# Optimization experiments

Measured on AMD Instinct MI355X. Metric: run time of the kernel, lower is better.

## Reference

```python
import jax, jax.numpy as jnp
import numpy as np

D_MODEL = 1024
NUM_HEADS = 16
HEAD_DIM = D_MODEL // NUM_HEADS
B, T = 4, 2048


def setup_inputs() -> dict:
    key = jax.random.key(0)
    ks = jax.random.split(key, 11)
    s = 0.02
    return {
        "q": jax.random.normal(ks[0], (B, T, D_MODEL), jnp.float32),
        "k": jax.random.normal(ks[1], (B, T, D_MODEL), jnp.float32),
        "v": jax.random.normal(ks[2], (B, T, D_MODEL), jnp.float32),
        "Wq": jax.random.normal(ks[3], (D_MODEL, D_MODEL), jnp.float32) * s,
        "bq": jnp.zeros((D_MODEL,), jnp.float32),
        "Wk": jax.random.normal(ks[4], (D_MODEL, D_MODEL), jnp.float32) * s,
        "bk": jnp.zeros((D_MODEL,), jnp.float32),
        "Wv": jax.random.normal(ks[5], (D_MODEL, D_MODEL), jnp.float32) * s,
        "bv": jnp.zeros((D_MODEL,), jnp.float32),
        "Wo": jax.random.normal(ks[6], (D_MODEL, D_MODEL), jnp.float32) * s,
        "bo": jnp.zeros((D_MODEL,), jnp.float32),
    }


def reference(q, k, v, Wq, bq, Wk, bk, Wv, bv, Wo, bo):
    Bq, Tq, _ = q.shape
    Tk = k.shape[1]
    # Linear projections then split heads: [B, H, T, Dh]
    qh = (q @ Wq + bq).reshape(Bq, Tq, NUM_HEADS, HEAD_DIM).transpose(0, 2, 1, 3)
    kh = (k @ Wk + bk).reshape(Bq, Tk, NUM_HEADS, HEAD_DIM).transpose(0, 2, 1, 3)
    vh = (v @ Wv + bv).reshape(Bq, Tk, NUM_HEADS, HEAD_DIM).transpose(0, 2, 1, 3)
    scale = 1.0 / jnp.sqrt(jnp.asarray(HEAD_DIM, qh.dtype))
    scores = jnp.einsum("bhqd,bhkd->bhqk", qh, kh) * scale  # [B,H,Tq,Tk]
    attn = jax.nn.softmax(scores, axis=-1)
    # dropout p=0.0 (eval) -> identity
    out = jnp.einsum("bhqk,bhkd->bhqd", attn, vh)  # [B,H,Tq,Dh]
    out = out.transpose(0, 2, 1, 3).reshape(Bq, Tq, D_MODEL)
    return out @ Wo + bo
```

## Files before the change

### kernel.cpp

```cpp
#include <hip/hip_runtime.h>
#include <cstdint>

#define DEV static __device__ __forceinline__

typedef unsigned short u16;
typedef unsigned int u32;
typedef __attribute__((ext_vector_type(8))) _Float16 half8;
typedef __attribute__((ext_vector_type(4))) float f32x4;
typedef __attribute__((ext_vector_type(4))) unsigned short u16x4;

DEV u16 f2h_bits(float f) {
  _Float16 h = (_Float16)f;
  union { _Float16 h; u16 u; } cv; cv.h = h; return cv.u;
}

DEV u32 pack2h(float a, float b) {
  union { __fp16 __attribute__((ext_vector_type(2))) h; u32 u; } cv;
  cv.h = __builtin_amdgcn_cvt_pkrtz(a, b);
  return cv.u;
}

#define EXP2 __builtin_amdgcn_exp2f

DEV void async_cp16(const void* g, void* l) {
  __builtin_amdgcn_global_load_lds(
      (const __attribute__((address_space(1))) void*)g,
      (__attribute__((address_space(3))) void*)l, 16, 0, 0);
}

__global__ void cvt_f16(const float4* __restrict__ in, u16* __restrict__ out) {
  const int i = blockIdx.x * 256 + threadIdx.x;
  float4 f = in[i];
  u16x4 u;
  u.x = f2h_bits(f.x); u.y = f2h_bits(f.y); u.z = f2h_bits(f.z); u.w = f2h_bits(f.w);
  *(u16x4*)(out + i * 4) = u;
}

struct TParams { const float* W[4]; u16* out[4]; };

__global__ void tcvt4(TParams p) {
  __shared__ float tile[32][33];
  const int w = blockIdx.x >> 10;
  const int bidx = blockIdx.x & 1023;
  const float* __restrict__ Wf = p.W[w];
  u16* __restrict__ Wt = p.out[w];
  const int bx = bidx & 31, by = bidx >> 5;
  const int tx = threadIdx.x & 31, ty = threadIdx.x >> 5;
#pragma unroll
  for (int r = 0; r < 32; r += 8)
    tile[ty + r][tx] = Wf[(by * 32 + ty + r) * 1024 + bx * 32 + tx];
  __syncthreads();
#pragma unroll
  for (int r = 0; r < 32; r += 8)
    Wt[(bx * 32 + ty + r) * 1024 + by * 32 + tx] = f2h_bits(tile[tx][ty + r]);
}

template<int EPI, typename OutT>
DEV void gemm_body(const u16* __restrict__ A, const u16* __restrict__ Bt,
                   const float* __restrict__ bias, OutT* __restrict__ out,
                   u16 (*As)[8192], u16 (*Bs)[8192])
{
  const int tid = threadIdx.x;
  const int wave = tid >> 6, lane = tid & 63;
  const int l15 = lane & 15, lg = lane >> 4;
  const int bid = ((blockIdx.x & 7) << 6) | (blockIdx.x >> 3);
  const int bm = bid >> 3, bn = bid & 7;
  const int m0 = bm * 128, n0 = bn * 128;
  const int wr = wave >> 1, wc = wave & 1;

  const f32x4 fz = {0.f, 0.f, 0.f, 0.f};
  f32x4 acc[4][4];
#pragma unroll
  for (int m = 0; m < 4; ++m)
#pragma unroll
    for (int n = 0; n < 4; ++n) acc[m][n] = fz;

  const char* srcA[4]; const char* srcB[4]; int dstAB[4];
#pragma unroll
  for (int j = 0; j < 4; ++j) {
    const int x = (j * 256 + tid) * 16;
    const int row = x >> 7, colb = x & 127;
    const int pc = colb ^ ((row & 7) << 4);
    srcA[j] = (const char*)A  + (size_t)(m0 + row) * 2048 + pc;
    srcB[j] = (const char*)Bt + (size_t)(n0 + row) * 2048 + pc;
    dstAB[j] = x;
  }

#define STAGE_G(buf, T)                                                     \
  do {                                                                      \
    _Pragma("unroll") for (int j = 0; j < 4; ++j)                           \
      async_cp16(srcA[j] + (size_t)(T) * 128, (char*)As[buf] + dstAB[j]);   \
    _Pragma("unroll") for (int j = 0; j < 4; ++j)                           \
      async_cp16(srcB[j] + (size_t)(T) * 128, (char*)Bs[buf] + dstAB[j]);   \
  } while (0)

  STAGE_G(0, 0);
  asm volatile("s_waitcnt vmcnt(0)" ::: "memory");
  __builtin_amdgcn_s_barrier();
  __builtin_amdgcn_sched_barrier(0);

#define GEMM_IT(T, BR, BS)                                                  \
  do {                                                                      \
    if ((T) < 15) STAGE_G(BS, (T) + 1);                                     \
    half8 af[2][4], bf[2][4];                                               \
    _Pragma("unroll") for (int kk = 0; kk < 2; ++kk)                        \
      _Pragma("unroll") for (int m = 0; m < 4; ++m) {                       \
        const int row = wr * 64 + m * 16 + l15;                             \
        af[kk][m] = *(const half8*)((const char*)As[BR] +                   \
            ((row * 128 + kk * 64 + lg * 16) ^ ((row & 7) << 4)));          \
      }                                                                     \
    _Pragma("unroll") for (int kk = 0; kk < 2; ++kk)                        \
      _Pragma("unroll") for (int n = 0; n < 4; ++n) {                       \
        const int row = wc * 64 + n * 16 + l15;                             \
        bf[kk][n] = *(const half8*)((const char*)Bs[BR] +                   \
            ((row * 128 + kk * 64 + lg * 16) ^ ((row & 7) << 4)));          \
      }                                                                     \
    _Pragma("unroll") for (int kk = 0; kk < 2; ++kk)                        \
      _Pragma("unroll") for (int m = 0; m < 4; ++m)                         \
        _Pragma("unroll") for (int n = 0; n < 4; ++n)                       \
          acc[m][n] = __builtin_amdgcn_mfma_f32_16x16x32_f16(af[kk][m], bf[kk][n], acc[m][n], 0, 0, 0); \
    if ((T) < 15) {                                                         \
      asm volatile("s_waitcnt vmcnt(0)" ::: "memory");                      \
      __builtin_amdgcn_s_barrier();                                         \
      __builtin_amdgcn_sched_barrier(0);                                    \
    }                                                                       \
  } while (0)

  for (int tb = 0; tb < 16; tb += 2) {
    GEMM_IT(tb,     0, 1);
    GEMM_IT(tb + 1, 1, 0);
  }
#undef GEMM_IT
#undef STAGE_G

#pragma unroll
  for (int m = 0; m < 4; ++m) {
    const int Rb = m0 + wr * 64 + m * 16 + lg * 4;
#pragma unroll
    for (int n = 0; n < 4; ++n) {
      const int C = n0 + wc * 64 + n * 16 + l15;
      const float bv = bias[C];
#pragma unroll
      for (int i = 0; i < 4; ++i) {
        const int R = Rb + i;
        const float vv = acc[m][n][i] + bv;
        if (EPI == 3) {
          ((float*)out)[(size_t)R * 1024 + C] = vv;
        } else {
          const int b = R >> 11, t = R & 2047, hh = C >> 6, d = C & 63;
          if (EPI == 0)
            ((u16*)out)[((b * 16 + hh) * 2048 + t) * 64 + d] = f2h_bits(vv * 0.18033688f);
          else if (EPI == 1)
            ((u16*)out)[((b * 16 + hh) * 2048 + t) * 64 + d] = f2h_bits(vv);
          else
            ((u16*)out)[((b * 16 + hh) * 64 + d) * 2048 + t] = f2h_bits(vv);
        }
      }
    }
  }
}

template<int EPI>
__launch_bounds__(256, 2)
__global__ void gemm_proj(const u16* __restrict__ A, const u16* __restrict__ Bt,
                          const float* __restrict__ bias, u16* __restrict__ out)
{
  __shared__ u16 As[2][8192];
  __shared__ u16 Bs[2][8192];
  gemm_body<EPI, u16>(A, Bt, bias, out, As, Bs);
}

__launch_bounds__(256, 2)
__global__ void gemm_o(const u16* __restrict__ A, const u16* __restrict__ Bt,
                       const float* __restrict__ bias, float* __restrict__ out)
{
  __shared__ u16 As[2][8192];
  __shared__ u16 Bs[2][8192];
  gemm_body<3, float>(A, Bt, bias, out, As, Bs);
}

__launch_bounds__(512)
__global__ void attn_kernel(const u16* __restrict__ qh, const u16* __restrict__ kh,
                            const u16* __restrict__ vt, u16* __restrict__ O)
{
  __shared__ u16 SM[16384];
  const int tid = threadIdx.x, wave = tid >> 6, lane = tid & 63;
  const int l15 = lane & 15, lg = lane >> 4;
  const int swz = ((blockIdx.x & 7) << 6) | (blockIdx.x >> 3);
  const int bh = swz >> 3;
  const int q0 = (swz & 7) << 8;
  const int b = bh >> 4, h = bh & 15;

  const char* qbase = (const char*)(qh + (size_t)(bh * 2048 + q0) * 64);
  const char* kbase = (const char*)(kh + (size_t)bh * 2048 * 64);
  const char* vbase = (const char*)(vt + (size_t)bh * 64 * 2048);

  char* Kbuf[2] = { (char*)SM,         (char*)SM + 8192 };
  char* Vbuf[2] = { (char*)SM + 16384, (char*)SM + 24576 };

  const bool isK = wave < 4;
  const char* ksrc[2]; int kdst[2];
  const char* vsrc[2]; int vdstA[2], vdstB[2];
#pragma unroll
  for (int j = 0; j < 2; ++j) {
    if (isK) {
      const int yb = wave * 2048 + j * 1024 + lane * 16;
      const int row = yb >> 7;
      ksrc[j] = kbase + (yb ^ ((row & 7) << 4));
      kdst[j] = yb;
      vsrc[j] = nullptr; vdstA[j] = vdstB[j] = 0;
    } else {
      const int u = (wave - 4) * 128 + j * 64 + lane;
      const int d = u >> 3, a = u & 7;
      vsrc[j] = vbase + (size_t)d * 4096 + a * 16;
      const int n = a >> 1;
      const int s1 = 32 * (n >> 1) + 16 * (a & 1) + 4 * (n & 1);
      const int sw = (d & 7) << 4;
      vdstA[j] = (d * 128 + 2 * s1) ^ sw;
      vdstB[j] = (d * 128 + 2 * s1 + 16) ^ sw;
      ksrc[j] = nullptr; kdst[j] = 0;
    }
  }

#pragma unroll
  for (int j = 0; j < 4; ++j) {
    const int x = j * 8192 + tid * 16;
    const int row = x >> 7;
    async_cp16(qbase + (x ^ ((row & 7) << 4)), (char*)SM + x);
  }
  __syncthreads();
  half8 aq[2][2];
#pragma unroll
  for (int G = 0; G < 2; ++G) {
    const int qr = wave * 32 + G * 16 + l15;
#pragma unroll
    for (int hh = 0; hh < 2; ++hh) {
      const int addr = (qr * 128 + hh * 64 + lg * 16) ^ ((qr & 7) << 4);
      aq[G][hh] = *(const half8*)((const char*)SM + addr);
    }
  }
  asm volatile("s_waitcnt lgkmcnt(0)" ::: "memory");
  __syncthreads();

  uint4 va[2];
  if (isK) {
    async_cp16(ksrc[0], Kbuf[0] + kdst[0]);
    async_cp16(ksrc[1], Kbuf[0] + kdst[1]);
    asm volatile("s_waitcnt vmcnt(0)" ::: "memory");
  } else {
#pragma unroll
    for (int j = 0; j < 2; ++j) {
      uint4 v = *(const uint4*)(vsrc[j]);
      uint2 w0; w0.x = v.x; w0.y = v.y;
      uint2 w1; w1.x = v.z; w1.y = v.w;
      *(uint2*)(Vbuf[0] + vdstA[j]) = w0;
      *(uint2*)(Vbuf[0] + vdstB[j]) = w1;
    }
#pragma unroll
    for (int j = 0; j < 2; ++j) va[j] = *(const uint4*)(vsrc[j] + 128);
    asm volatile("s_waitcnt lgkmcnt(0)" ::: "memory");
  }
  __builtin_amdgcn_s_barrier();
  __builtin_amdgcn_sched_barrier(0);

  half8 ones;
#pragma unroll
  for (int i = 0; i < 8; ++i) ones[i] = (_Float16)1.0f;

  const f32x4 fz = {0.f, 0.f, 0.f, 0.f};
  f32x4 o[4][2], osum[2];
#pragma unroll
  for (int i = 0; i < 4; ++i) { o[i][0] = fz; o[i][1] = fz; }
  osum[0] = fz; osum[1] = fz;

#define ATTN_IT(T, BR, BS)                                                      \
  do {                                                                          \
    const int t_ = (T);                                                         \
    if (isK) {                                                                  \
      if (t_ < 31) {                                                            \
        async_cp16(ksrc[0] + (size_t)(t_ + 1) * 8192, Kbuf[BS] + kdst[0]);      \
        async_cp16(ksrc[1] + (size_t)(t_ + 1) * 8192, Kbuf[BS] + kdst[1]);      \
      }                                                                         \
    } else {                                                                    \
      if (t_ < 31) {                                                            \
        _Pragma("unroll") for (int j = 0; j < 2; ++j) {                         \
          uint2 w0; w0.x = va[j].x; w0.y = va[j].y;                             \
          uint2 w1; w1.x = va[j].z; w1.y = va[j].w;                             \
          *(uint2*)(Vbuf[BS] + vdstA[j]) = w0;                                  \
          *(uint2*)(Vbuf[BS] + vdstB[j]) = w1;                                  \
        }                                                                       \
        if (t_ < 30) {                                                          \
          _Pragma("unroll") for (int j = 0; j < 2; ++j)                         \
            va[j] = *(const uint4*)(vsrc[j] + (size_t)(t_ + 2) * 128);          \
        }                                                                       \
      }                                                                         \
    }                                                                           \
    f32x4 s[4][2];                                                              \
    __builtin_amdgcn_s_setprio(1);                                              \
    _Pragma("unroll") for (int n = 0; n < 4; ++n) {                             \
      const int krow = n * 16 + l15;                                            \
      const int a0 = (krow * 128 + lg * 16) ^ ((krow & 7) << 4);                \
      half8 bk0 = *(const half8*)(Kbuf[BR] + a0);                               \
      half8 bk1 = *(const half8*)(Kbuf[BR] + (a0 ^ 64));                        \
      s[n][0] = __builtin_amdgcn_mfma_f32_16x16x32_f16(bk0, aq[0][0], fz, 0, 0, 0); \
      s[n][0] = __builtin_amdgcn_mfma_f32_16x16x32_f16(bk1, aq[0][1], s[n][0], 0, 0, 0); \
      s[n][1] = __builtin_amdgcn_mfma_f32_16x16x32_f16(bk0, aq[1][0], fz, 0, 0, 0); \
      s[n][1] = __builtin_amdgcn_mfma_f32_16x16x32_f16(bk1, aq[1][1], s[n][1], 0, 0, 0); \
    }                                                                           \
    __builtin_amdgcn_s_setprio(0);                                              \
    half8 pa[2][2];                                                             \
    _Pragma("unroll") for (int G = 0; G < 2; ++G)                               \
      _Pragma("unroll") for (int hh = 0; hh < 2; ++hh) {                        \
        union { u32 w[4]; half8 hv; } cv;                                       \
        cv.w[0] = pack2h(EXP2(s[2*hh][G][0]),   EXP2(s[2*hh][G][1]));           \
        cv.w[1] = pack2h(EXP2(s[2*hh][G][2]),   EXP2(s[2*hh][G][3]));           \
        cv.w[2] = pack2h(EXP2(s[2*hh+1][G][0]), EXP2(s[2*hh+1][G][1]));         \
        cv.w[3] = pack2h(EXP2(s[2*hh+1][G][2]), EXP2(s[2*hh+1][G][3]));         \
        pa[G][hh] = cv.hv;                                                      \
      }                                                                         \
    __builtin_amdgcn_s_setprio(1);                                              \
    _Pragma("unroll") for (int G = 0; G < 2; ++G) {                             \
      osum[G] = __builtin_amdgcn_mfma_f32_16x16x32_f16(pa[G][0], ones, osum[G], 0, 0, 0); \
      osum[G] = __builtin_amdgcn_mfma_f32_16x16x32_f16(pa[G][1], ones, osum[G], 0, 0, 0); \
    }                                                                           \
    _Pragma("unroll") for (int nd = 0; nd < 4; ++nd) {                          \
      const int dr = nd * 16 + l15;                                             \
      const int a0 = (dr * 128 + lg * 16) ^ ((dr & 7) << 4);                    \
      half8 bv0 = *(const half8*)(Vbuf[BR] + a0);                               \
      half8 bv1 = *(const half8*)(Vbuf[BR] + (a0 ^ 64));                        \
      o[nd][0] = __builtin_amdgcn_mfma_f32_16x16x32_f16(pa[0][0], bv0, o[nd][0], 0, 0, 0); \
      o[nd][0] = __builtin_amdgcn_mfma_f32_16x16x32_f16(pa[0][1], bv1, o[nd][0], 0, 0, 0); \
      o[nd][1] = __builtin_amdgcn_mfma_f32_16x16x32_f16(pa[1][0], bv0, o[nd][1], 0, 0, 0); \
      o[nd][1] = __builtin_amdgcn_mfma_f32_16x16x32_f16(pa[1][1], bv1, o[nd][1], 0, 0, 0); \
    }                                                                           \
    __builtin_amdgcn_s_setprio(0);                                              \
    if (t_ < 31) {                                                              \
      if (isK) asm volatile("s_waitcnt vmcnt(0)" ::: "memory");                 \
      else     asm volatile("s_waitcnt lgkmcnt(0)" ::: "memory");               \
      __builtin_amdgcn_s_barrier();                                             \
      __builtin_amdgcn_sched_barrier(0);                                        \
    }                                                                           \
  } while (0)

  for (int tb = 0; tb < 32; tb += 2) {
    ATTN_IT(tb,     0, 1);
    ATTN_IT(tb + 1, 1, 0);
  }
#undef ATTN_IT

#pragma unroll
  for (int G = 0; G < 2; ++G)
#pragma unroll
    for (int i = 0; i < 4; ++i) {
      const float inv = 1.f / osum[G][i];
      const int t = q0 + wave * 32 + G * 16 + lg * 4 + i;
      u16* orow = O + ((size_t)(b * 2048 + t)) * 1024 + h * 64;
#pragma unroll
      for (int nd = 0; nd < 4; ++nd)
        orow[nd * 16 + l15] = f2h_bits(o[nd][G][i] * inv);
    }
}

extern "C" void kernel_launch(void* const* d_in, const int* in_sizes, int n_in,
                              void* d_out, int out_size, void* d_ws, size_t ws_size,
                              hipStream_t stream)
{
  const float* q  = (const float*)d_in[0];
  const float* k  = (const float*)d_in[1];
  const float* v  = (const float*)d_in[2];
  const float* Wq = (const float*)d_in[3];
  const float* bq = (const float*)d_in[4];
  const float* Wk = (const float*)d_in[5];
  const float* bk = (const float*)d_in[6];
  const float* Wv = (const float*)d_in[7];
  const float* bv = (const float*)d_in[8];
  const float* Wo = (const float*)d_in[9];
  const float* bo = (const float*)d_in[10];

  u16* W = (u16*)d_ws;
  const unsigned MB = 1u << 20;
  u16* wtq = W + 0 * MB;
  u16* wtk = W + 1 * MB;
  u16* wtv = W + 2 * MB;
  u16* wto = W + 3 * MB;
  u16* qhb = W + 4 * MB;
  u16* khb = W + 12 * MB;
  u16* vtb = W + 20 * MB;
  u16* Xb  = W + 28 * MB;

  TParams tp;
  tp.W[0] = Wq; tp.W[1] = Wk; tp.W[2] = Wv; tp.W[3] = Wo;
  tp.out[0] = wtq; tp.out[1] = wtk; tp.out[2] = wtv; tp.out[3] = wto;
  tcvt4<<<4096, 256, 0, stream>>>(tp);

  cvt_f16<<<8192, 256, 0, stream>>>((const float4*)q, Xb);
  gemm_proj<0><<<512, 256, 0, stream>>>(Xb, wtq, bq, qhb);
  cvt_f16<<<8192, 256, 0, stream>>>((const float4*)k, Xb);
  gemm_proj<1><<<512, 256, 0, stream>>>(Xb, wtk, bk, khb);
  cvt_f16<<<8192, 256, 0, stream>>>((const float4*)v, Xb);
  gemm_proj<2><<<512, 256, 0, stream>>>(Xb, wtv, bv, vtb);

  attn_kernel<<<512, 512, 0, stream>>>(qhb, khb, vtb, Xb);

  gemm_o<<<512, 256, 0, stream>>>(Xb, wto, bo, (float*)d_out);
}
```

Baseline: 205.2 us.

## Stage two K/V tiles per barrier period with quad-buffered shared memory

The attention loop now processes two KV tiles per synchronisation period, using four K and four V buffers in shared memory instead of two. Loads for the next pair of tiles are issued while the current pair is computed. This halves the number of block-wide barriers and waits per KV sweep. In exchange, LDS use doubles to 64KB per block, which may reduce occupancy, and more registers are needed for the V prefetch.

```diff
diff --git a/kernel.cpp b/kernel.cpp
--- a/kernel.cpp
+++ b/kernel.cpp
@@ -183,7 +183,7 @@
 __global__ void attn_kernel(const u16* __restrict__ qh, const u16* __restrict__ kh,
                             const u16* __restrict__ vt, u16* __restrict__ O)
 {
-  __shared__ u16 SM[16384];
+  __shared__ u16 SM[32768];
   const int tid = threadIdx.x, wave = tid >> 6, lane = tid & 63;
   const int l15 = lane & 15, lg = lane >> 4;
   const int swz = ((blockIdx.x & 7) << 6) | (blockIdx.x >> 3);
@@ -195,8 +195,10 @@
   const char* kbase = (const char*)(kh + (size_t)bh * 2048 * 64);
   const char* vbase = (const char*)(vt + (size_t)bh * 64 * 2048);
 
-  char* Kbuf[2] = { (char*)SM,         (char*)SM + 8192 };
-  char* Vbuf[2] = { (char*)SM + 16384, (char*)SM + 24576 };
+  char* Kbuf[4] = { (char*)SM,         (char*)SM + 8192,
+                    (char*)SM + 16384, (char*)SM + 24576 };
+  char* Vbuf[4] = { (char*)SM + 32768, (char*)SM + 40960,
+                    (char*)SM + 49152, (char*)SM + 57344 };
 
   const bool isK = wave < 4;
   const char* ksrc[2]; int kdst[2];
@@ -242,22 +244,29 @@
   asm volatile("s_waitcnt lgkmcnt(0)" ::: "memory");
   __syncthreads();
 
-  uint4 va[2];
+  uint4 va[2][2];
   if (isK) {
     async_cp16(ksrc[0], Kbuf[0] + kdst[0]);
     async_cp16(ksrc[1], Kbuf[0] + kdst[1]);
+    async_cp16(ksrc[0] + 8192, Kbuf[1] + kdst[0]);
+    async_cp16(ksrc[1] + 8192, Kbuf[1] + kdst[1]);
     asm volatile("s_waitcnt vmcnt(0)" ::: "memory");
   } else {
 #pragma unroll
+    for (int tt = 0; tt < 2; ++tt)
+#pragma unroll
+      for (int j = 0; j < 2; ++j) {
+        uint4 v = *(const uint4*)(vsrc[j] + (size_t)tt * 128);
+        uint2 w0; w0.x = v.x; w0.y = v.y;
+        uint2 w1; w1.x = v.z; w1.y = v.w;
+        *(uint2*)(Vbuf[tt] + vdstA[j]) = w0;
+        *(uint2*)(Vbuf[tt] + vdstB[j]) = w1;
+      }
+#pragma unroll
     for (int j = 0; j < 2; ++j) {
-      uint4 v = *(const uint4*)(vsrc[j]);
-      uint2 w0; w0.x = v.x; w0.y = v.y;
-      uint2 w1; w1.x = v.z; w1.y = v.w;
-      *(uint2*)(Vbuf[0] + vdstA[j]) = w0;
-      *(uint2*)(Vbuf[0] + vdstB[j]) = w1;
+      va[0][j] = *(const uint4*)(vsrc[j] + 2 * 128);
+      va[1][j] = *(const uint4*)(vsrc[j] + 3 * 128);
     }
-#pragma unroll
-    for (int j = 0; j < 2; ++j) va[j] = *(const uint4*)(vsrc[j] + 128);
     asm volatile("s_waitcnt lgkmcnt(0)" ::: "memory");
   }
   __builtin_amdgcn_s_barrier();
@@ -273,35 +282,15 @@
   for (int i = 0; i < 4; ++i) { o[i][0] = fz; o[i][1] = fz; }
   osum[0] = fz; osum[1] = fz;
 
-#define ATTN_IT(T, BR, BS)                                                      \
+#define ATTN_TILE(BT)                                                           \
   do {                                                                          \
-    const int t_ = (T);                                                         \
-    if (isK) {                                                                  \
-      if (t_ < 31) {                                                            \
-        async_cp16(ksrc[0] + (size_t)(t_ + 1) * 8192, Kbuf[BS] + kdst[0]);      \
-        async_cp16(ksrc[1] + (size_t)(t_ + 1) * 8192, Kbuf[BS] + kdst[1]);      \
-      }                                                                         \
-    } else {                                                                    \
-      if (t_ < 31) {                                                            \
-        _Pragma("unroll") for (int j = 0; j < 2; ++j) {                         \
-          uint2 w0; w0.x = va[j].x; w0.y = va[j].y;                             \
-          uint2 w1; w1.x = va[j].z; w1.y = va[j].w;                             \
-          *(uint2*)(Vbuf[BS] + vdstA[j]) = w0;                                  \
-          *(uint2*)(Vbuf[BS] + vdstB[j]) = w1;                                  \
-        }                                                                       \
-        if (t_ < 30) {                                                          \
-          _Pragma("unroll") for (int j = 0; j < 2; ++j)                         \
-            va[j] = *(const uint4*)(vsrc[j] + (size_t)(t_ + 2) * 128);          \
-        }                                                                       \
-      }                                                                         \
-    }                                                                           \
     f32x4 s[4][2];                                                              \
     __builtin_amdgcn_s_setprio(1);                                              \
     _Pragma("unroll") for (int n = 0; n < 4; ++n) {                             \
       const int krow = n * 16 + l15;                                            \
       const int a0 = (krow * 128 + lg * 16) ^ ((krow & 7) << 4);                \
-      half8 bk0 = *(const half8*)(Kbuf[BR] + a0);                               \
-      half8 bk1 = *(const half8*)(Kbuf[BR] + (a0 ^ 64));                        \
+      half8 bk0 = *(const half8*)(Kbuf[BT] + a0);                               \
+      half8 bk1 = *(const half8*)(Kbuf[BT] + (a0 ^ 64));                        \
       s[n][0] = __builtin_amdgcn_mfma_f32_16x16x32_f16(bk0, aq[0][0], fz, 0, 0, 0); \
       s[n][0] = __builtin_amdgcn_mfma_f32_16x16x32_f16(bk1, aq[0][1], s[n][0], 0, 0, 0); \
       s[n][1] = __builtin_amdgcn_mfma_f32_16x16x32_f16(bk0, aq[1][0], fz, 0, 0, 0); \
@@ -326,15 +315,49 @@
     _Pragma("unroll") for (int nd = 0; nd < 4; ++nd) {                          \
       const int dr = nd * 16 + l15;                                             \
       const int a0 = (dr * 128 + lg * 16) ^ ((dr & 7) << 4);                    \
-      half8 bv0 = *(const half8*)(Vbuf[BR] + a0);                               \
-      half8 bv1 = *(const half8*)(Vbuf[BR] + (a0 ^ 64));                        \
+      half8 bv0 = *(const half8*)(Vbuf[BT] + a0);                               \
+      half8 bv1 = *(const half8*)(Vbuf[BT] + (a0 ^ 64));                        \
       o[nd][0] = __builtin_amdgcn_mfma_f32_16x16x32_f16(pa[0][0], bv0, o[nd][0], 0, 0, 0); \
       o[nd][0] = __builtin_amdgcn_mfma_f32_16x16x32_f16(pa[0][1], bv1, o[nd][0], 0, 0, 0); \
       o[nd][1] = __builtin_amdgcn_mfma_f32_16x16x32_f16(pa[1][0], bv0, o[nd][1], 0, 0, 0); \
       o[nd][1] = __builtin_amdgcn_mfma_f32_16x16x32_f16(pa[1][1], bv1, o[nd][1], 0, 0, 0); \
     }                                                                           \
     __builtin_amdgcn_s_setprio(0);                                              \
-    if (t_ < 31) {                                                              \
+  } while (0)
+
+#define PERIOD(P, C0, C1, S0, S1, DOSTAGE, DOVA, DOBAR)                         \
+  do {                                                                          \
+    if (isK) {                                                                  \
+      if (DOSTAGE) {                                                            \
+        async_cp16(ksrc[0] + (size_t)(2*(P)+2) * 8192, Kbuf[S0] + kdst[0]);     \
+        async_cp16(ksrc[1] + (size_t)(2*(P)+2) * 8192, Kbuf[S0] + kdst[1]);     \
+        async_cp16(ksrc[0] + (size_t)(2*(P)+3) * 8192, Kbuf[S1] + kdst[0]);     \
+        async_cp16(ksrc[1] + (size_t)(2*(P)+3) * 8192, Kbuf[S1] + kdst[1]);     \
+      }                                                                         \
+    } else {                                                                    \
+      if (DOSTAGE) {                                                            \
+        _Pragma("unroll") for (int j = 0; j < 2; ++j) {                         \
+          uint2 w0, w1;                                                         \
+          w0.x = va[0][j].x; w0.y = va[0][j].y;                                 \
+          w1.x = va[0][j].z; w1.y = va[0][j].w;                                 \
+          *(uint2*)(Vbuf[S0] + vdstA[j]) = w0;                                  \
+          *(uint2*)(Vbuf[S0] + vdstB[j]) = w1;                                  \
+          w0.x = va[1][j].x; w0.y = va[1][j].y;                                 \
+          w1.x = va[1][j].z; w1.y = va[1][j].w;                                 \
+          *(uint2*)(Vbuf[S1] + vdstA[j]) = w0;                                  \
+          *(uint2*)(Vbuf[S1] + vdstB[j]) = w1;                                  \
+        }                                                                       \
+        if (DOVA) {                                                             \
+          _Pragma("unroll") for (int j = 0; j < 2; ++j) {                       \
+            va[0][j] = *(const uint4*)(vsrc[j] + (size_t)(2*(P)+4) * 128);      \
+            va[1][j] = *(const uint4*)(vsrc[j] + (size_t)(2*(P)+5) * 128);      \
+          }                                                                     \
+        }                                                                       \
+      }                                                                         \
+    }                                                                           \
+    ATTN_TILE(C0);                                                              \
+    ATTN_TILE(C1);                                                              \
+    if (DOBAR) {                                                                \
       if (isK) asm volatile("s_waitcnt vmcnt(0)" ::: "memory");                 \
       else     asm volatile("s_waitcnt lgkmcnt(0)" ::: "memory");               \
       __builtin_amdgcn_s_barrier();                                             \
@@ -342,11 +365,14 @@
     }                                                                           \
   } while (0)
 
-  for (int tb = 0; tb < 32; tb += 2) {
-    ATTN_IT(tb,     0, 1);
-    ATTN_IT(tb + 1, 1, 0);
-  }
-#undef ATTN_IT
+  for (int pb = 0; pb < 14; pb += 2) {
+    PERIOD(pb,     0, 1, 2, 3, 1, 1, 1);
+    PERIOD(pb + 1, 2, 3, 0, 1, 1, 1, 1);
+  }
+  PERIOD(14, 0, 1, 2, 3, 1, 0, 1);
+  PERIOD(15, 2, 3, 0, 1, 0, 0, 0);
+#undef PERIOD
+#undef ATTN_TILE
 
 #pragma unroll
   for (int G = 0; G < 2; ++G)
```

After: 204.6 us. Within noise of the previous version (-0.3%).
